# Kernel tuning notes

Measured on AMD Instinct MI355X. Metric: run time of the kernel, lower is better.

Reference implementation:

```python
import jax, jax.numpy as jnp
import numpy as np
from jax import lax


def setup_inputs() -> dict:
    key = jax.random.key(0)
    I = jax.random.uniform(key, (32, 3, 512, 512), dtype=jnp.float32)
    return {"I": I, "k": 15}


def reference(I, k):
    # Channel-wise min -> dark channel (torch does this via -max_pool over transposed channel dim)
    dark = jnp.min(I, axis=1, keepdims=True)  # [B,1,H,W]
    p = k // 2
    # Spatial min-pool kxk, stride 1, pad k//2. torch max_pool2d pads with -inf,
    # so the min-pool equivalent pads with +inf: reduce_window with min and +inf init.
    eroded = lax.reduce_window(
        dark,
        jnp.inf,
        lax.min,
        window_dimensions=(1, 1, k, k),
        window_strides=(1, 1, 1, 1),
        padding=[(0, 0), (0, 0), (p, p), (p, p)],
    )
    return eroded
```

## Files before the change

### kernel.cpp

```cpp
#include <hip/hip_runtime.h>
#include <math.h>

#define BATCH  32
#define CH     3
#define H      512
#define W      512
#define KWIN   15
#define PAD    7
#define TH     16
#define NRR    (TH + KWIN - 1)
#define STRIP  112
#define NSTRIP 5
#define NWAVES (BATCH * (H / TH) * NSTRIP)
#define DEPTH  5

static __device__ __forceinline__ float2 min2(float2 a, float2 b) {
    float2 r;
    r.x = fminf(a.x, b.x);
    r.y = fminf(a.y, b.y);
    return r;
}

__global__ void dcp_fused8(const float* __restrict__ I, float* __restrict__ out) {
    const int wid = blockIdx.x * 4 + (threadIdx.x >> 6);
    const int L   = threadIdx.x & 63;
    const int s   = wid % NSTRIP;
    const int rb  = (wid / NSTRIP) % (H / TH);
    const int b   = wid / (NSTRIP * (H / TH));
    const int y0  = rb * TH;
    const int f   = s * STRIP - 8 + 2 * L;
    const int cl  = min(max(f, 0), W - 2);
    const bool cv = (f >= 0) && (f < W);
    const bool st = (L >= 4) && (L <= 59) && (f < W);

    const float* base = I + (size_t)b * CH * H * W + cl;
    float* outb = out + (size_t)b * H * W;

    auto seqrow = [](int q) { return q < KWIN ? KWIN + q : 29 - q; };

    auto loadrow = [&](int i, float2& A, float2& B, float2& C) {
        const int yc = min(max(y0 - PAD + i, 0), H - 1);
        const float* p = base + (size_t)yc * W;
        A = *(const float2*)(p);
        B = *(const float2*)(p + (size_t)H * W);
        C = *(const float2*)(p + (size_t)2 * H * W);
    };

    auto hcompute = [&](int i, float2 A, float2 B, float2 C) -> float2 {
        const int y = y0 - PAD + i;
        float2 d = min2(min2(A, B), C);
        const bool pad = (y < 0) || (y >= H) || !cv;
        d.x = pad ? INFINITY : d.x;
        d.y = pad ? INFINITY : d.y;
        const float pm = fminf(d.x, d.y);
        const float t2 = fminf(pm, __shfl_down(pm, 1));
        const float t4 = fminf(t2, __shfl_down(t2, 2));
        const float q7 = fminf(t4, __shfl_up(t4, 3));
        float2 wv;
        wv.x = fminf(q7, __shfl_up(d.y, 4));
        wv.y = fminf(q7, __shfl_down(d.x, 4));
        return wv;
    };

    float2 Ab[DEPTH], Bb[DEPTH], Cb[DEPTH];
    #pragma unroll
    for (int j = 0; j < DEPTH; ++j)
        loadrow(seqrow(j), Ab[j], Bb[j], Cb[j]);

    float2 P[KWIN];
    float2 U;
    #pragma unroll
    for (int q = 0; q < NRR; ++q) {
        const int sl = q % DEPTH;
        const float2 h = hcompute(seqrow(q), Ab[sl], Bb[sl], Cb[sl]);
        if (q + DEPTH < NRR)
            loadrow(seqrow(q + DEPTH), Ab[sl], Bb[sl], Cb[sl]);

        if (q == 0) {
            P[0] = h;
        } else if (q < KWIN) {
            P[q] = min2(P[q - 1], h);
            if (q == KWIN - 1 && st)
                *(float2*)(outb + (size_t)(y0 + 15) * W + f) = P[KWIN - 1];
        } else if (q == KWIN) {
            U = h;
            if (st) *(float2*)(outb + (size_t)(y0 + 14) * W + f) = min2(U, P[13]);
        } else if (q < NRR - 1) {
            const int r = 29 - q;
            U = min2(U, h);
            if (st) *(float2*)(outb + (size_t)(y0 + r) * W + f) = min2(U, P[r - 1]);
        } else {
            U = min2(U, h);
            if (st) *(float2*)(outb + (size_t)y0 * W + f) = U;
        }
    }
}

extern "C" void kernel_launch(void* const* d_in, const int* in_sizes, int n_in,
                              void* d_out, int out_size, void* d_ws, size_t ws_size,
                              hipStream_t stream) {
    const float* I = (const float*)d_in[0];
    float* out = (float*)d_out;
    dcp_fused8<<<dim3(NWAVES / 4), dim3(256), 0, stream>>>(I, out);
}
```

Baseline: 159.2 us.

## Widen per-lane columns to float4 and use three wider strips per row band

Each lane now handles four adjacent columns with float4 loads and stores instead of two, so a wavefront covers a 240-column strip and three strips span the row instead of five. The horizontal 15-wide min is rebuilt from per-lane prefix and suffix mins plus neighbour shuffles at distance 1 and 2. This cuts the redundant halo columns loaded per strip and the number of wavefronts, and uses wider memory transactions. In exchange it needs more registers per thread, leaves fewer waves in flight, and the prefetch depth drops from five to four.

```diff
diff --git a/kernel.cpp b/kernel.cpp
--- a/kernel.cpp
+++ b/kernel.cpp
@@ -9,89 +9,105 @@
 #define PAD    7
 #define TH     16
 #define NRR    (TH + KWIN - 1)
-#define STRIP  112
-#define NSTRIP 5
+#define STRIP  240
+#define NSTRIP 3
 #define NWAVES (BATCH * (H / TH) * NSTRIP)
-#define DEPTH  5
+#define DEPTH  4
 
-static __device__ __forceinline__ float2 min2(float2 a, float2 b) {
-    float2 r;
+static __device__ __forceinline__ float4 min4(float4 a, float4 b) {
+    float4 r;
     r.x = fminf(a.x, b.x);
     r.y = fminf(a.y, b.y);
+    r.z = fminf(a.z, b.z);
+    r.w = fminf(a.w, b.w);
     return r;
 }
 
-__global__ void dcp_fused8(const float* __restrict__ I, float* __restrict__ out) {
+__global__ void dcp_fused9(const float* __restrict__ I, float* __restrict__ out) {
     const int wid = blockIdx.x * 4 + (threadIdx.x >> 6);
     const int L   = threadIdx.x & 63;
     const int s   = wid % NSTRIP;
     const int rb  = (wid / NSTRIP) % (H / TH);
     const int b   = wid / (NSTRIP * (H / TH));
     const int y0  = rb * TH;
-    const int f   = s * STRIP - 8 + 2 * L;
-    const int cl  = min(max(f, 0), W - 2);
+    const int f   = s * STRIP - 8 + 4 * L;
+    const int cl  = min(max(f, 0), W - 4);
     const bool cv = (f >= 0) && (f < W);
-    const bool st = (L >= 4) && (L <= 59) && (f < W);
+    const bool st = (L >= 2) && (L <= 61) && (f <= W - 4);
 
     const float* base = I + (size_t)b * CH * H * W + cl;
     float* outb = out + (size_t)b * H * W;
 
     auto seqrow = [](int q) { return q < KWIN ? KWIN + q : 29 - q; };
 
-    auto loadrow = [&](int i, float2& A, float2& B, float2& C) {
+    auto loadrow = [&](int i, float4& A, float4& B, float4& C) {
         const int yc = min(max(y0 - PAD + i, 0), H - 1);
         const float* p = base + (size_t)yc * W;
-        A = *(const float2*)(p);
-        B = *(const float2*)(p + (size_t)H * W);
-        C = *(const float2*)(p + (size_t)2 * H * W);
+        A = *(const float4*)(p);
+        B = *(const float4*)(p + (size_t)H * W);
+        C = *(const float4*)(p + (size_t)2 * H * W);
     };
 
-    auto hcompute = [&](int i, float2 A, float2 B, float2 C) -> float2 {
+    auto hcompute = [&](int i, float4 A, float4 B, float4 C) -> float4 {
         const int y = y0 - PAD + i;
-        float2 d = min2(min2(A, B), C);
+        float4 d = min4(min4(A, B), C);
         const bool pad = (y < 0) || (y >= H) || !cv;
         d.x = pad ? INFINITY : d.x;
         d.y = pad ? INFINITY : d.y;
-        const float pm = fminf(d.x, d.y);
-        const float t2 = fminf(pm, __shfl_down(pm, 1));
-        const float t4 = fminf(t2, __shfl_down(t2, 2));
-        const float q7 = fminf(t4, __shfl_up(t4, 3));
-        float2 wv;
-        wv.x = fminf(q7, __shfl_up(d.y, 4));
-        wv.y = fminf(q7, __shfl_down(d.x, 4));
+        d.z = pad ? INFINITY : d.z;
+        d.w = pad ? INFINITY : d.w;
+        const float p01  = fminf(d.x, d.y);
+        const float p23  = fminf(d.z, d.w);
+        const float m    = fminf(p01, p23);
+        const float pre3 = fminf(p01, d.z);
+        const float suf3 = fminf(d.y, p23);
+        const float mL   = __shfl_up(m, 1);
+        const float mR   = __shfl_down(m, 1);
+        const float cmn  = fminf(fminf(mL, mR), m);
+        const float s1   = __shfl_up(d.w, 2);
+        const float s2   = __shfl_up(p23, 2);
+        const float s3   = __shfl_up(suf3, 2);
+        const float q1   = __shfl_down(d.x, 2);
+        const float q2   = __shfl_down(p01, 2);
+        const float q3   = __shfl_down(pre3, 2);
+        float4 wv;
+        wv.x = fminf(cmn, s3);
+        wv.y = fminf(fminf(s2, q1), cmn);
+        wv.z = fminf(fminf(s1, q2), cmn);
+        wv.w = fminf(cmn, q3);
         return wv;
     };
 
-    float2 Ab[DEPTH], Bb[DEPTH], Cb[DEPTH];
+    float4 Ab[DEPTH], Bb[DEPTH], Cb[DEPTH];
     #pragma unroll
     for (int j = 0; j < DEPTH; ++j)
         loadrow(seqrow(j), Ab[j], Bb[j], Cb[j]);
 
-    float2 P[KWIN];
-    float2 U;
+    float4 P[KWIN];
+    float4 U;
     #pragma unroll
     for (int q = 0; q < NRR; ++q) {
         const int sl = q % DEPTH;
-        const float2 h = hcompute(seqrow(q), Ab[sl], Bb[sl], Cb[sl]);
+        const float4 h = hcompute(seqrow(q), Ab[sl], Bb[sl], Cb[sl]);
         if (q + DEPTH < NRR)
             loadrow(seqrow(q + DEPTH), Ab[sl], Bb[sl], Cb[sl]);
 
         if (q == 0) {
             P[0] = h;
         } else if (q < KWIN) {
-            P[q] = min2(P[q - 1], h);
+            P[q] = min4(P[q - 1], h);
             if (q == KWIN - 1 && st)
-                *(float2*)(outb + (size_t)(y0 + 15) * W + f) = P[KWIN - 1];
+                *(float4*)(outb + (size_t)(y0 + 15) * W + f) = P[KWIN - 1];
         } else if (q == KWIN) {
             U = h;
-            if (st) *(float2*)(outb + (size_t)(y0 + 14) * W + f) = min2(U, P[13]);
+            if (st) *(float4*)(outb + (size_t)(y0 + 14) * W + f) = min4(U, P[13]);
         } else if (q < NRR - 1) {
             const int r = 29 - q;
-            U = min2(U, h);
-            if (st) *(float2*)(outb + (size_t)(y0 + r) * W + f) = min2(U, P[r - 1]);
+            U = min4(U, h);
+            if (st) *(float4*)(outb + (size_t)(y0 + r) * W + f) = min4(U, P[r - 1]);
         } else {
-            U = min2(U, h);
-            if (st) *(float2*)(outb + (size_t)y0 * W + f) = U;
+            U = min4(U, h);
+            if (st) *(float4*)(outb + (size_t)y0 * W + f) = U;
         }
     }
 }
@@ -101,5 +117,5 @@
                               hipStream_t stream) {
     const float* I = (const float*)d_in[0];
     float* out = (float*)d_out;
-    dcp_fused8<<<dim3(NWAVES / 4), dim3(256), 0, stream>>>(I, out);
+    dcp_fused9<<<dim3(NWAVES / 4), dim3(256), 0, stream>>>(I, out);
 }
```

Measured after the change: 168.7 us. 5.9% more time.

## Share horizontal min rows across waves via LDS with taller row tiles

Applied to the files above, without the earlier changes.

Each block now covers 64 output rows of a strip. Its four waves cooperatively compute the channel-min and horizontal 15-wide min for the 78 needed rows and store them in shared memory. After a barrier, each wave does the vertical pass for its 16 rows from LDS. The intent is to cut redundant loads and horizontal work: the halo overhead drops from 30/16 to 78/64 rows per output row. In exchange it adds LDS traffic, a block-wide sync, less load pipelining depth and fewer blocks.

```diff
diff --git a/kernel.cpp b/kernel.cpp
--- a/kernel.cpp
+++ b/kernel.cpp
@@ -7,12 +7,12 @@
 #define W      512
 #define KWIN   15
 #define PAD    7
-#define TH     16
-#define NRR    (TH + KWIN - 1)
+#define TB     64
+#define NR     (TB + KWIN - 1)
 #define STRIP  112
 #define NSTRIP 5
-#define NWAVES (BATCH * (H / TH) * NSTRIP)
-#define DEPTH  5
+#define LROW   112
+#define NBLK   (BATCH * (H / TB) * NSTRIP)
 
 static __device__ __forceinline__ float2 min2(float2 a, float2 b) {
     float2 r;
@@ -21,35 +21,37 @@
     return r;
 }
 
-__global__ void dcp_fused8(const float* __restrict__ I, float* __restrict__ out) {
-    const int wid = blockIdx.x * 4 + (threadIdx.x >> 6);
+__global__ void dcp_lds1(const float* __restrict__ I, float* __restrict__ out) {
+    __shared__ float hl[NR][LROW];
+
+    const int w   = threadIdx.x >> 6;
     const int L   = threadIdx.x & 63;
-    const int s   = wid % NSTRIP;
-    const int rb  = (wid / NSTRIP) % (H / TH);
-    const int b   = wid / (NSTRIP * (H / TH));
-    const int y0  = rb * TH;
+    const int bid = blockIdx.x;
+    const int s   = bid % NSTRIP;
+    const int rg  = (bid / NSTRIP) % (H / TB);
+    const int b   = bid / (NSTRIP * (H / TB));
+    const int Y0  = rg * TB;
+
     const int f   = s * STRIP - 8 + 2 * L;
     const int cl  = min(max(f, 0), W - 2);
     const bool cv = (f >= 0) && (f < W);
-    const bool st = (L >= 4) && (L <= 59) && (f < W);
+    const bool sw = (L >= 4) && (L <= 59);
 
     const float* base = I + (size_t)b * CH * H * W + cl;
     float* outb = out + (size_t)b * H * W;
 
-    auto seqrow = [](int q) { return q < KWIN ? KWIN + q : 29 - q; };
-
-    auto loadrow = [&](int i, float2& A, float2& B, float2& C) {
-        const int yc = min(max(y0 - PAD + i, 0), H - 1);
-        const float* p = base + (size_t)yc * W;
+    auto ldrow = [&](int j, float2& A, float2& B, float2& C) {
+        const int gc = min(max(Y0 - PAD + j, 0), H - 1);
+        const float* p = base + (size_t)gc * W;
         A = *(const float2*)(p);
         B = *(const float2*)(p + (size_t)H * W);
         C = *(const float2*)(p + (size_t)2 * H * W);
     };
 
-    auto hcompute = [&](int i, float2 A, float2 B, float2 C) -> float2 {
-        const int y = y0 - PAD + i;
+    auto hrow = [&](int j, float2 A, float2 B, float2 C) -> float2 {
+        const int g = Y0 - PAD + j;
         float2 d = min2(min2(A, B), C);
-        const bool pad = (y < 0) || (y >= H) || !cv;
+        const bool pad = (g < 0) || (g >= H) || !cv;
         d.x = pad ? INFINITY : d.x;
         d.y = pad ? INFINITY : d.y;
         const float pm = fminf(d.x, d.y);
@@ -62,36 +64,58 @@
         return wv;
     };
 
-    float2 Ab[DEPTH], Bb[DEPTH], Cb[DEPTH];
+    float2 Ab[4], Bb[4], Cb[4];
     #pragma unroll
-    for (int j = 0; j < DEPTH; ++j)
-        loadrow(seqrow(j), Ab[j], Bb[j], Cb[j]);
+    for (int t = 0; t < 4; ++t)
+        ldrow(w + 4 * t, Ab[t], Bb[t], Cb[t]);
+
+    #pragma unroll
+    for (int t = 0; t < 20; ++t) {
+        const int j = w + 4 * t;
+        if (j < NR) {
+            const int sl = t & 3;
+            const float2 hv = hrow(j, Ab[sl], Bb[sl], Cb[sl]);
+            const int j2 = w + 4 * (t + 4);
+            if (t + 4 < 20 && j2 < NR)
+                ldrow(j2, Ab[sl], Bb[sl], Cb[sl]);
+            if (sw)
+                *(float2*)&hl[j][2 * L - 8] = hv;
+        }
+    }
+    __syncthreads();
+
+    const int lw = 16 * w;
+    const int c  = min(2 * L, LROW - 2);
+    const int oc = s * STRIP + 2 * L;
+    const bool st = (2 * L < LROW) && (oc < W);
+
+    auto seqrow = [](int q) { return q < KWIN ? KWIN + q : 29 - q; };
+    auto rdrow  = [&](int l) -> float2 {
+        return *(const float2*)&hl[lw + l][c];
+    };
 
     float2 P[KWIN];
     float2 U;
     #pragma unroll
-    for (int q = 0; q < NRR; ++q) {
-        const int sl = q % DEPTH;
-        const float2 h = hcompute(seqrow(q), Ab[sl], Bb[sl], Cb[sl]);
-        if (q + DEPTH < NRR)
-            loadrow(seqrow(q + DEPTH), Ab[sl], Bb[sl], Cb[sl]);
-
+    for (int q = 0; q < 30; ++q) {
+        const int l = seqrow(q);
+        const float2 h = rdrow(l);
         if (q == 0) {
             P[0] = h;
         } else if (q < KWIN) {
             P[q] = min2(P[q - 1], h);
             if (q == KWIN - 1 && st)
-                *(float2*)(outb + (size_t)(y0 + 15) * W + f) = P[KWIN - 1];
+                *(float2*)(outb + (size_t)(Y0 + lw + 15) * W + oc) = P[KWIN - 1];
         } else if (q == KWIN) {
             U = h;
-            if (st) *(float2*)(outb + (size_t)(y0 + 14) * W + f) = min2(U, P[13]);
-        } else if (q < NRR - 1) {
+            if (st) *(float2*)(outb + (size_t)(Y0 + lw + 14) * W + oc) = min2(U, P[13]);
+        } else if (q < 29) {
             const int r = 29 - q;
             U = min2(U, h);
-            if (st) *(float2*)(outb + (size_t)(y0 + r) * W + f) = min2(U, P[r - 1]);
+            if (st) *(float2*)(outb + (size_t)(Y0 + lw + r) * W + oc) = min2(U, P[r - 1]);
         } else {
             U = min2(U, h);
-            if (st) *(float2*)(outb + (size_t)y0 * W + f) = U;
+            if (st) *(float2*)(outb + (size_t)(Y0 + lw) * W + oc) = U;
         }
     }
 }
@@ -101,5 +125,5 @@
                               hipStream_t stream) {
     const float* I = (const float*)d_in[0];
     float* out = (float*)d_out;
-    dcp_fused8<<<dim3(NWAVES / 4), dim3(256), 0, stream>>>(I, out);
+    dcp_lds1<<<dim3(NBLK), dim3(256), 0, stream>>>(I, out);
 }
```

Measured after the change: 159.8 us. About the same (+0.3%).

## Stage input rows into LDS via async global_load_lds shared by four waves

Applied to the files above, without the earlier changes.

Replaces per-wave register row loads with block-level asynchronous global-to-LDS copies (global_load_lds) in a 4-slot ring, staging 8 rows of 3 channels per chunk over a 64-row block band. Each wave consumes the shared staged rows for its 16-row output tile, so the 14-row vertical halo is loaded once per block instead of once per wave, cutting redundant global reads. It adds block barriers, manual vmcnt waits and LDS usage, which may reduce occupancy and serialize waves on barriers.

```diff
diff --git a/kernel.cpp b/kernel.cpp
--- a/kernel.cpp
+++ b/kernel.cpp
@@ -7,12 +7,12 @@
 #define W      512
 #define KWIN   15
 #define PAD    7
-#define TH     16
-#define NRR    (TH + KWIN - 1)
+#define TB     64
+#define NCHK   10
 #define STRIP  112
 #define NSTRIP 5
-#define NWAVES (BATCH * (H / TH) * NSTRIP)
-#define DEPTH  5
+#define NBLK   (BATCH * (H / TB) * NSTRIP)
+#define SLOT_F (8 * 3 * 128)
 
 static __device__ __forceinline__ float2 min2(float2 a, float2 b) {
     float2 r;
@@ -21,37 +21,58 @@
     return r;
 }
 
-__global__ void dcp_fused8(const float* __restrict__ I, float* __restrict__ out) {
-    const int wid = blockIdx.x * 4 + (threadIdx.x >> 6);
+__global__ void dcp_dma1(const float* __restrict__ I, float* __restrict__ out) {
+    __shared__ float raw[4 * SLOT_F];
+
+    const int w   = threadIdx.x >> 6;
     const int L   = threadIdx.x & 63;
-    const int s   = wid % NSTRIP;
-    const int rb  = (wid / NSTRIP) % (H / TH);
-    const int b   = wid / (NSTRIP * (H / TH));
-    const int y0  = rb * TH;
+    const int bid = blockIdx.x;
+    const int s   = bid % NSTRIP;
+    const int rg  = (bid / NSTRIP) % (H / TB);
+    const int b   = bid / (NSTRIP * (H / TB));
+    const int Y0  = rg * TB;
+
+    const int q    = L & 31;
+    const int g    = L >> 5;
+    const int gq   = s * STRIP - 8 + 4 * q;
+    const int gcl4 = min(max(gq, 0), W - 4);
+
     const int f   = s * STRIP - 8 + 2 * L;
-    const int cl  = min(max(f, 0), W - 2);
     const bool cv = (f >= 0) && (f < W);
     const bool st = (L >= 4) && (L <= 59) && (f < W);
 
-    const float* base = I + (size_t)b * CH * H * W + cl;
+    const float* Ib = I + (size_t)b * CH * H * W;
     float* outb = out + (size_t)b * H * W;
 
-    auto seqrow = [](int q) { return q < KWIN ? KWIN + q : 29 - q; };
-
-    auto loadrow = [&](int i, float2& A, float2& B, float2& C) {
-        const int yc = min(max(y0 - PAD + i, 0), H - 1);
-        const float* p = base + (size_t)yc * W;
-        A = *(const float2*)(p);
-        B = *(const float2*)(p + (size_t)H * W);
-        C = *(const float2*)(p + (size_t)2 * H * W);
+    auto stage = [&](int k) {
+        const int slot = k & 3;
+        #pragma unroll
+        for (int i = 0; i < 3; ++i) {
+            const int m  = 3 * w + i;
+            const int p  = 2 * m + g;
+            const int ch = p % 3;
+            const int jr = p / 3;
+            const int j  = 8 * k + jr;
+            const int y  = min(max(Y0 - PAD + j, 0), H - 1);
+            const float* gp = Ib + (size_t)ch * H * W + (size_t)y * W + gcl4;
+            float* lp = &raw[slot * SLOT_F + m * 256];
+            __builtin_amdgcn_global_load_lds(
+                (const __attribute__((address_space(1))) void*)gp,
+                (__attribute__((address_space(3))) void*)lp,
+                16, 0, 0);
+        }
     };
 
-    auto hcompute = [&](int i, float2 A, float2 B, float2 C) -> float2 {
-        const int y = y0 - PAD + i;
-        float2 d = min2(min2(A, B), C);
-        const bool pad = (y < 0) || (y >= H) || !cv;
-        d.x = pad ? INFINITY : d.x;
-        d.y = pad ? INFINITY : d.y;
+    auto hrowL = [&](int slot, int jr, int j) -> float2 {
+        const int fb = slot * SLOT_F + jr * 384 + 2 * L;
+        const float2 A  = *(const float2*)&raw[fb];
+        const float2 Bv = *(const float2*)&raw[fb + 128];
+        const float2 Cv = *(const float2*)&raw[fb + 256];
+        float2 d = min2(min2(A, Bv), Cv);
+        const int gy = Y0 - PAD + j;
+        const bool bad = (gy < 0) || (gy >= H) || !cv;
+        d.x = bad ? INFINITY : d.x;
+        d.y = bad ? INFINITY : d.y;
         const float pm = fminf(d.x, d.y);
         const float t2 = fminf(pm, __shfl_down(pm, 1));
         const float t4 = fminf(t2, __shfl_down(t2, 2));
@@ -62,37 +83,69 @@
         return wv;
     };
 
-    float2 Ab[DEPTH], Bb[DEPTH], Cb[DEPTH];
+    float2 hbuf[15];
+    float2 obuf[16];
+    float2 R;
+    R.x = INFINITY; R.y = INFINITY;
+
+    stage(0);
+    stage(1);
+
     #pragma unroll
-    for (int j = 0; j < DEPTH; ++j)
-        loadrow(seqrow(j), Ab[j], Bb[j], Cb[j]);
+    for (int k = 0; k < NCHK; ++k) {
+        if (k + 2 < NCHK) stage(k + 2);
+        if (k < 8)       asm volatile("s_waitcnt vmcnt(6)" ::: "memory");
+        else if (k == 8) asm volatile("s_waitcnt vmcnt(3)" ::: "memory");
+        else             asm volatile("s_waitcnt vmcnt(0)" ::: "memory");
+        __builtin_amdgcn_sched_barrier(0);
+        __builtin_amdgcn_s_barrier();
+        __builtin_amdgcn_sched_barrier(0);
 
-    float2 P[KWIN];
-    float2 U;
-    #pragma unroll
-    for (int q = 0; q < NRR; ++q) {
-        const int sl = q % DEPTH;
-        const float2 h = hcompute(seqrow(q), Ab[sl], Bb[sl], Cb[sl]);
-        if (q + DEPTH < NRR)
-            loadrow(seqrow(q + DEPTH), Ab[sl], Bb[sl], Cb[sl]);
+        const int slot = k & 3;
+        const int e = k - 2 * w;
+        if (e == 0) {
+            #pragma unroll
+            for (int t = 0; t < 8; ++t)
+                hbuf[t] = hrowL(slot, t, 16 * w + t);
+        } else if (e == 1) {
+            #pragma unroll
+            for (int t = 8; t < 16; ++t) {
+                const float2 h = hrowL(slot, t - 8, 16 * w + t);
+                if (t < 14) {
+                    hbuf[t] = h;
+                } else if (t == 14) {
+                    hbuf[14] = h;
+                    #pragma unroll
+                    for (int u = 13; u >= 0; --u)
+                        hbuf[u] = min2(hbuf[u], hbuf[u + 1]);
+                    obuf[0] = hbuf[0];
+                } else {
+                    R = h;
+                    obuf[1] = min2(hbuf[1], R);
+                }
+            }
+        } else if (e == 2) {
+            #pragma unroll
+            for (int t = 16; t < 24; ++t) {
+                const float2 h = hrowL(slot, t - 16, 16 * w + t);
+                R = min2(R, h);
+                obuf[t - 14] = min2(hbuf[t - 14], R);
+            }
+        } else if (e == 3) {
+            #pragma unroll
+            for (int t = 24; t < 30; ++t) {
+                const float2 h = hrowL(slot, t - 24, 16 * w + t);
+                R = min2(R, h);
+                if (t < 29) obuf[t - 14] = min2(hbuf[t - 14], R);
+                else        obuf[15] = R;
+            }
+        }
+    }
 
-        if (q == 0) {
-            P[0] = h;
-        } else if (q < KWIN) {
-            P[q] = min2(P[q - 1], h);
-            if (q == KWIN - 1 && st)
-                *(float2*)(outb + (size_t)(y0 + 15) * W + f) = P[KWIN - 1];
-        } else if (q == KWIN) {
-            U = h;
-            if (st) *(float2*)(outb + (size_t)(y0 + 14) * W + f) = min2(U, P[13]);
-        } else if (q < NRR - 1) {
-            const int r = 29 - q;
-            U = min2(U, h);
-            if (st) *(float2*)(outb + (size_t)(y0 + r) * W + f) = min2(U, P[r - 1]);
-        } else {
-            U = min2(U, h);
-            if (st) *(float2*)(outb + (size_t)y0 * W + f) = U;
-        }
+    if (st) {
+        #pragma unroll
+        for (int r = 0; r < 16; ++r)
+            *(float2*)(outb + (size_t)(Y0 + 16 * w + r) * W + f) = obuf[r];
     }
 }
 
@@ -101,5 +154,5 @@
                               hipStream_t stream) {
     const float* I = (const float*)d_in[0];
     float* out = (float*)d_out;
-    dcp_fused8<<<dim3(NWAVES / 4), dim3(256), 0, stream>>>(I, out);
+    dcp_dma1<<<dim3(NBLK), dim3(256), 0, stream>>>(I, out);
 }
```

New measurement: 167.0 us. 4.9% more time.
